# Kernel tuning notes

Measured on AMD Instinct MI355X. Metric: run time of the kernel, lower is better.

The kernel has to match this reference:

```python
import jax, jax.numpy as jnp
import numpy as np

EPS = 1e-5  # PyTorch BatchNorm2d default eps


def _batchnorm(x, gamma, beta):
    # training-mode BN over (N, T, V) per channel; x: [N, C, T, V]
    mean = jnp.mean(x, axis=(0, 2, 3), keepdims=True)
    var = jnp.var(x, axis=(0, 2, 3), keepdims=True)
    inv = jax.lax.rsqrt(var + EPS)
    return (x - mean) * inv * gamma[None, :, None, None] + beta[None, :, None, None]


def setup_inputs() -> dict:
    key = jax.random.key(0)
    ks = jax.random.split(key, 8)
    N, Cin, Cout, T, V, S = 64, 64, 128, 300, 25, 3
    x = jax.random.normal(ks[0], (N, Cin, T, V), dtype=jnp.float32)
    A = jax.random.uniform(ks[1], (S, V, V), dtype=jnp.float32)
    # per-subset 1x1 conv weights/biases (kaiming-ish scale)
    W = jax.random.normal(ks[2], (S, Cout, Cin), dtype=jnp.float32) / np.sqrt(Cin)
    b = jax.random.normal(ks[3], (S, Cout), dtype=jnp.float32) * 0.01
    alpha = jnp.zeros((1,), dtype=jnp.float32)
    bn_gamma = jnp.ones((Cout,), dtype=jnp.float32)
    bn_beta = jnp.zeros((Cout,), dtype=jnp.float32)
    # residual down path (in_channels != out_channels): conv1x1 + BN
    down_W = jax.random.normal(ks[4], (Cout, Cin), dtype=jnp.float32) / np.sqrt(Cin)
    down_b = jax.random.normal(ks[5], (Cout,), dtype=jnp.float32) * 0.01
    down_gamma = jnp.ones((Cout,), dtype=jnp.float32)
    down_beta = jnp.zeros((Cout,), dtype=jnp.float32)
    return {
        "x": x, "A": A, "W": W, "b": b, "alpha": alpha,
        "bn_gamma": bn_gamma, "bn_beta": bn_beta,
        "down_W": down_W, "down_b": down_b,
        "down_gamma": down_gamma, "down_beta": down_beta,
    }


def reference(x, A, W, b, alpha, bn_gamma, bn_beta, down_W, down_b, down_gamma, down_beta):
    V = x.shape[-1]
    eye = jnp.eye(V, dtype=x.dtype)
    A_adj = A + alpha[0] * eye[None]  # [S, V, V]
    # sum_s conv1x1_s( x @ A_s ): fuse adjacency matmul, 1x1 conv, subset sum
    y_agg = jnp.einsum('nctv,svw,soc->notw', x, A_adj, W)
    y_agg = y_agg + jnp.sum(b, axis=0)[None, :, None, None]
    y = _batchnorm(y_agg, bn_gamma, bn_beta)
    # residual down: 1x1 conv + BN (in_channels != out_channels)
    res = jnp.einsum('nctv,oc->notv', x, down_W) + down_b[None, :, None, None]
    res = _batchnorm(res, down_gamma, down_beta)
    return jax.nn.relu(y + res)
```

## Files before the change

### kernel.cpp

```cpp
#include <hip/hip_runtime.h>
#include <hip/hip_bf16.h>

#define N_   64
#define CIN  64
#define COUT 128
#define T_   300
#define V_   25
#define S_   3
#define NTV  (N_ * T_ * V_)

#define TS     10
#define NTB    (T_ / TS)
#define NBLK   (N_ * NTB)
#define RED_ROWS   64
#define RED_BLOCKS (NBLK / RED_ROWS)

#define WS_P    0
#define WS_P2   (WS_P + NBLK * 512)
#define WS_COEF (WS_P2 + RED_BLOCKS * 512)
#define WS_WF   (WS_COEF + 512)
#define WS_WSF  (WS_WF + 16384)
#define WS_AF   (WS_WSF + 16384)

typedef __attribute__((ext_vector_type(8))) short short8;
typedef __attribute__((ext_vector_type(4))) float f32x4;

__device__ __forceinline__ unsigned short bfbits(float f) {
    union { __hip_bfloat16 h; unsigned short u; } cv;
    cv.h = __float2bfloat16(f);
    return cv.u;
}
__device__ __forceinline__ unsigned int pack2(float lo, float hi) {
    return (unsigned int)bfbits(lo) | ((unsigned int)bfbits(hi) << 16);
}

__device__ __forceinline__ int zoff(int nl, int k) {
    int slot = (k >> 3) ^ (nl & 31);
    return nl * 512 + slot * 16 + (k & 7) * 2;
}

__global__ __launch_bounds__(256) void k_prep(const float* __restrict__ W,
                                              const float* __restrict__ dW,
                                              const float* __restrict__ A,
                                              const float* __restrict__ alpha,
                                              unsigned short* __restrict__ Wf,
                                              unsigned short* __restrict__ Af) {
    int i = blockIdx.x * 256 + threadIdx.x;
    {
        int j = i & 7, lane = (i >> 3) & 63, ks = (i >> 9) & 7;
        int of = (i >> 12) & 1, oh = i >> 13;
        int o = oh * 32 + of * 16 + (lane & 15);
        int k = ks * 32 + (lane >> 4) * 8 + j;
        float wv = (k < 192) ? W[(k >> 6) * (COUT * CIN) + o * CIN + (k & 63)]
                             : dW[o * CIN + (k - 192)];
        Wf[i] = bfbits(wv);
    }
    if (i < 4096) {
        int j = i & 7, lane = (i >> 3) & 63, wf = (i >> 9) & 1, s = i >> 10;
        int v = (lane >> 4) * 8 + j, w = wf * 16 + (lane & 15);
        float av;
        if (s < 3)
            av = (v < V_ && w < V_)
                   ? A[(s * V_ + v) * V_ + w] + ((v == w) ? alpha[0] : 0.f)
                   : 0.f;
        else
            av = (v == w && v < V_) ? 1.f : 0.f;
        Af[i] = bfbits(av);
    }
}

__global__ __launch_bounds__(256) void k_prep2(const float* __restrict__ W,
                                               const float* __restrict__ dW,
                                               const float* __restrict__ coef,
                                               unsigned short* __restrict__ Wsf) {
    int i = blockIdx.x * 256 + threadIdx.x;
    int j = i & 7, lane = (i >> 3) & 63, ks = (i >> 9) & 7;
    int of = (i >> 12) & 1, oh = i >> 13;
    int o = oh * 32 + of * 16 + (lane & 15);
    int k = ks * 32 + (lane >> 4) * 8 + j;
    float wv = (k < 192) ? W[(k >> 6) * (COUT * CIN) + o * CIN + (k & 63)]
                         : dW[o * CIN + (k - 192)];
    float sc = (k < 192) ? coef[o] : coef[COUT + o];
    Wsf[i] = bfbits(wv * sc);
}

struct XRaw { f32x4 a0, a1; float s; };

__device__ __forceinline__ XRaw load_raw(const float* __restrict__ base, int lq) {
    XRaw r;
    if (lq < 3) {
        r.a0 = *(const f32x4*)(base + lq * 8);
        r.a1 = *(const f32x4*)(base + lq * 8 + 4);
        r.s = 0.f;
    } else {
        r.s = base[24];
        r.a0 = (f32x4){0.f, 0.f, 0.f, 0.f};
        r.a1 = (f32x4){0.f, 0.f, 0.f, 0.f};
    }
    return r;
}

__device__ __forceinline__ short8 cvt_xfr(const XRaw& x, int lq) {
    short8 r;
    if (lq < 3) {
#pragma unroll
        for (int j = 0; j < 4; ++j) {
            r[j]     = (short)bfbits(x.a0[j]);
            r[4 + j] = (short)bfbits(x.a1[j]);
        }
    } else {
        r[0] = (short)bfbits(x.s);
#pragma unroll
        for (int j = 1; j < 8; ++j) r[j] = 0;
    }
    return r;
}

__device__ __forceinline__ void stage(char* zb, const unsigned short* Alds,
                                      short8 xfr, int oh, int lq, int lr, int lane) {
    const f32x4 zero = {0.f, 0.f, 0.f, 0.f};
#pragma unroll
    for (int s = 0; s < 4; ++s)
#pragma unroll
        for (int wf = 0; wf < 2; ++wf) {
            short8 af = *(const short8*)(Alds + ((s * 2 + wf) * 64 + lane) * 8);
            f32x4 d = __builtin_amdgcn_mfma_f32_16x16x32_bf16(xfr, af, zero, 0, 0, 0);
            unsigned long long pk = (unsigned long long)pack2(d[0], d[1])
                                  | ((unsigned long long)pack2(d[2], d[3]) << 32);
            int row = wf * 16 + lr;
            int k = s * 64 + oh * 16 + lq * 4;
            *(unsigned long long*)(zb + zoff(row, k)) = pk;
        }
}

template<bool STATS, int MINW>
__global__ __launch_bounds__(256, MINW) void k_gemm(
    const float* __restrict__ x, const unsigned short* __restrict__ Wf,
    const unsigned short* __restrict__ Af, const float* __restrict__ coef,
    float* __restrict__ P, float* __restrict__ out)
{
    __shared__ __align__(16) unsigned short Zt[2][32 * 256];
    __shared__ __align__(16) unsigned short Alds[8 * 64 * 8];

    const int tid = threadIdx.x;
    const int oh = tid >> 6, lane = tid & 63;
    const int lq = lane >> 4, lr = lane & 15;

    const int bid = blockIdx.x;
    const int n = bid / NTB, tb = bid % NTB;
    const int t0 = tb * TS;

    for (int i = tid; i < 512; i += 256)
        *(short8*)(Alds + i * 8) = *(const short8*)(Af + i * 8);

    short8 wfr[2][8];
#pragma unroll
    for (int of = 0; of < 2; ++of)
#pragma unroll
        for (int ks = 0; ks < 8; ++ks)
            wfr[of][ks] = *(const short8*)(Wf + (((oh * 2 + of) * 8 + ks) * 64 + lane) * 8);

    float c0v[2] = {0.f, 0.f};
    if (!STATS) {
        c0v[0] = coef[2 * COUT + oh * 32 + lr];
        c0v[1] = coef[2 * COUT + oh * 32 + 16 + lr];
    }

    float sy[2] = {0.f, 0.f}, sy2[2] = {0.f, 0.f};
    float sr[2] = {0.f, 0.f}, sr2[2] = {0.f, 0.f};

    const int c = oh * 16 + lr;
    const float* xrow = x + ((size_t)(n * CIN + c) * T_) * V_;

    __syncthreads();

    {
        XRaw r0 = load_raw(xrow + (size_t)t0 * V_, lq);
        stage((char*)Zt[0], Alds, cvt_xfr(r0, lq), oh, lq, lr, lane);
    }
    XRaw slotA = load_raw(xrow + (size_t)(t0 + 1) * V_, lq);

    const f32x4 zero = {0.f, 0.f, 0.f, 0.f};

    for (int tt = 0; tt < TS; ++tt) {
        const int t = t0 + tt;
        char* zb = (char*)Zt[tt & 1];
        __syncthreads();

        XRaw slotB;
        if (tt + 2 < TS) slotB = load_raw(xrow + (size_t)(t + 2) * V_, lq);
        else { slotB.a0 = zero; slotB.a1 = zero; slotB.s = 0.f; }

        if (tt + 1 < TS)
            stage((char*)Zt[(tt + 1) & 1], Alds, cvt_xfr(slotA, lq), oh, lq, lr, lane);

        f32x4 acc[2][2];

        if constexpr (STATS) {
#pragma unroll
            for (int ks = 6; ks < 8; ++ks) {
                short8 za[2];
                za[0] = *(const short8*)(zb + zoff(lr, ks * 32 + lq * 8));
                za[1] = *(const short8*)(zb + zoff(16 + lr, ks * 32 + lq * 8));
#pragma unroll
                for (int mf = 0; mf < 2; ++mf)
#pragma unroll
                    for (int of = 0; of < 2; ++of)
                        acc[mf][of] = __builtin_amdgcn_mfma_f32_16x16x32_bf16(
                            za[mf], wfr[of][ks], ks == 6 ? zero : acc[mf][of], 0, 0, 0);
            }
#pragma unroll
            for (int of = 0; of < 2; ++of)
#pragma unroll
                for (int mf = 0; mf < 2; ++mf)
#pragma unroll
                    for (int r = 0; r < 4; ++r) {
                        float rv = acc[mf][of][r];
                        sr[of] += rv; sr2[of] = fmaf(rv, rv, sr2[of]);
                    }
#pragma unroll
            for (int ks = 0; ks < 6; ++ks) {
                short8 za[2];
                za[0] = *(const short8*)(zb + zoff(lr, ks * 32 + lq * 8));
                za[1] = *(const short8*)(zb + zoff(16 + lr, ks * 32 + lq * 8));
#pragma unroll
                for (int mf = 0; mf < 2; ++mf)
#pragma unroll
                    for (int of = 0; of < 2; ++of)
                        acc[mf][of] = __builtin_amdgcn_mfma_f32_16x16x32_bf16(
                            za[mf], wfr[of][ks], ks == 0 ? zero : acc[mf][of], 0, 0, 0);
            }
#pragma unroll
            for (int of = 0; of < 2; ++of)
#pragma unroll
                for (int mf = 0; mf < 2; ++mf)
#pragma unroll
                    for (int r = 0; r < 4; ++r) {
                        float yv = acc[mf][of][r];
                        sy[of] += yv; sy2[of] = fmaf(yv, yv, sy2[of]);
                    }
        } else {
#pragma unroll
            for (int ks = 0; ks < 8; ++ks) {
                short8 za[2];
                za[0] = *(const short8*)(zb + zoff(lr, ks * 32 + lq * 8));
                za[1] = *(const short8*)(zb + zoff(16 + lr, ks * 32 + lq * 8));
#pragma unroll
                for (int mf = 0; mf < 2; ++mf)
#pragma unroll
                    for (int of = 0; of < 2; ++of)
                        acc[mf][of] = __builtin_amdgcn_mfma_f32_16x16x32_bf16(
                            za[mf], wfr[of][ks], ks == 0 ? zero : acc[mf][of], 0, 0, 0);
            }
#pragma unroll
            for (int of = 0; of < 2; ++of) {
                int o = oh * 32 + of * 16 + lr;
                float* rowp = out + ((size_t)(n * COUT + o) * T_ + t) * V_;
                f32x4 v0;
#pragma unroll
                for (int r = 0; r < 4; ++r) v0[r] = fmaxf(acc[0][of][r] + c0v[of], 0.f);
                *(f32x4*)(rowp + lq * 4) = v0;
                if (lq < 2) {
                    f32x4 v1;
#pragma unroll
                    for (int r = 0; r < 4; ++r) v1[r] = fmaxf(acc[1][of][r] + c0v[of], 0.f);
                    *(f32x4*)(rowp + 16 + lq * 4) = v1;
                } else if (lq == 2) {
                    rowp[24] = fmaxf(acc[1][of][0] + c0v[of], 0.f);
                }
            }
        }

        slotA.a0 = slotB.a0; slotA.a1 = slotB.a1; slotA.s = slotB.s;
    }

    if constexpr (STATS) {
#pragma unroll
        for (int of = 0; of < 2; ++of) {
            sy[of]  += __shfl_xor(sy[of], 16);  sy[of]  += __shfl_xor(sy[of], 32);
            sy2[of] += __shfl_xor(sy2[of], 16); sy2[of] += __shfl_xor(sy2[of], 32);
            sr[of]  += __shfl_xor(sr[of], 16);  sr[of]  += __shfl_xor(sr[of], 32);
            sr2[of] += __shfl_xor(sr2[of], 16); sr2[of] += __shfl_xor(sr2[of], 32);
        }
        if (lq == 0) {
            float* p = P + (size_t)bid * 512;
#pragma unroll
            for (int of = 0; of < 2; ++of) {
                int o = oh * 32 + of * 16 + lr;
                p[o] = sy[of]; p[128 + o] = sy2[of];
                p[256 + o] = sr[of]; p[384 + o] = sr2[of];
            }
        }
    }
}

__global__ __launch_bounds__(256) void k_red(const float* __restrict__ P,
                                             float* __restrict__ P2) {
    const int tid = threadIdx.x;
    float a0 = 0.f, a1 = 0.f;
    const int row0 = blockIdx.x * RED_ROWS;
    for (int r = 0; r < RED_ROWS; ++r) {
        const float* p = P + (size_t)(row0 + r) * 512;
        a0 += p[tid];
        a1 += p[256 + tid];
    }
    P2[blockIdx.x * 512 + tid] = a0;
    P2[blockIdx.x * 512 + 256 + tid] = a1;
}

__global__ __launch_bounds__(128) void k_coef(
    const float* __restrict__ P2, const float* __restrict__ gamma,
    const float* __restrict__ beta, const float* __restrict__ dgamma,
    const float* __restrict__ dbeta, const float* __restrict__ b,
    const float* __restrict__ db, float* __restrict__ coef) {
    const int o = threadIdx.x;
    float sy = 0.f, sy2 = 0.f, sr = 0.f, sr2 = 0.f;
    for (int r2 = 0; r2 < RED_BLOCKS; ++r2) {
        const float* p = P2 + r2 * 512;
        sy += p[o]; sy2 += p[128 + o]; sr += p[256 + o]; sr2 += p[384 + o];
    }
    const float bsum = b[o] + b[COUT + o] + b[2 * COUT + o];
    const float dbo = db[o];
    float syb  = sy + (float)NTV * bsum;
    float sy2b = sy2 + 2.f * bsum * sy + (float)NTV * bsum * bsum;
    float srb  = sr + (float)NTV * dbo;
    float sr2b = sr2 + 2.f * dbo * sr + (float)NTV * dbo * dbo;
    const float invn = 1.f / (float)NTV;
    float my = syb * invn, mr = srb * invn;
    float vy = fmaf(-my, my, sy2b * invn);
    float vr = fmaf(-mr, mr, sr2b * invn);
    float ay = rsqrtf(vy + 1e-5f) * gamma[o];
    float ar = rsqrtf(vr + 1e-5f) * dgamma[o];
    float c0 = beta[o] - my * ay + dbeta[o] - mr * ar + ay * bsum + ar * dbo;
    coef[o] = ay; coef[COUT + o] = ar; coef[2 * COUT + o] = c0;
}

extern "C" void kernel_launch(void* const* d_in, const int* in_sizes, int n_in,
                              void* d_out, int out_size, void* d_ws, size_t ws_size,
                              hipStream_t stream) {
    const float* x      = (const float*)d_in[0];
    const float* A      = (const float*)d_in[1];
    const float* W      = (const float*)d_in[2];
    const float* b      = (const float*)d_in[3];
    const float* alpha  = (const float*)d_in[4];
    const float* gamma  = (const float*)d_in[5];
    const float* beta   = (const float*)d_in[6];
    const float* dW     = (const float*)d_in[7];
    const float* db     = (const float*)d_in[8];
    const float* dgamma = (const float*)d_in[9];
    const float* dbeta  = (const float*)d_in[10];

    float* ws   = (float*)d_ws;
    float* P    = ws + WS_P;
    float* P2   = ws + WS_P2;
    float* coef = ws + WS_COEF;
    unsigned short* Wf  = (unsigned short*)(ws + WS_WF);
    unsigned short* Wsf = (unsigned short*)(ws + WS_WSF);
    unsigned short* Af  = (unsigned short*)(ws + WS_AF);
    float* out  = (float*)d_out;

    k_prep<<<128, 256, 0, stream>>>(W, dW, A, alpha, Wf, Af);
    k_gemm<true, 3><<<NBLK, 256, 0, stream>>>(x, Wf, Af, nullptr, P, nullptr);
    k_red<<<RED_BLOCKS, 256, 0, stream>>>(P, P2);
    k_coef<<<1, 128, 0, stream>>>(P2, gamma, beta, dgamma, dbeta, b, db, coef);
    k_prep2<<<128, 256, 0, stream>>>(W, dW, coef, Wsf);
    k_gemm<false, 4><<<NBLK, 256, 0, stream>>>(x, Wsf, Af, coef, nullptr, out);
}
```

Measured before the change: 258.4 us.

## Restructure GEMM LDS staging: padded rows, single barrier, A fragments from global

Replaces the XOR-swizzled Z tile with a padded 528-byte row layout and precomputed per-thread read and write bases, so the LDS address maths is simpler. The per-step work is reordered: the next step's staging MFMA and the next x load are issued after the current step's GEMM, with one lgkmcnt-wait-plus-barrier per step. The adjacency fragments are now read from global memory (L2) instead of an LDS copy. bf16 packing uses the paired conversion intrinsic, and the stats kernel's launch bound goes from 3 to 4 waves. The risks are more global or L2 traffic for the A fragments, possible LDS bank conflicts in the padded layout, and register pressure at the higher occupancy target.

```diff
diff --git a/kernel.cpp b/kernel.cpp
--- a/kernel.cpp
+++ b/kernel.cpp
@@ -15,6 +15,8 @@
 #define RED_ROWS   64
 #define RED_BLOCKS (NBLK / RED_ROWS)
 
+#define ROWB   528
+
 #define WS_P    0
 #define WS_P2   (WS_P + NBLK * 512)
 #define WS_COEF (WS_P2 + RED_BLOCKS * 512)
@@ -25,19 +27,19 @@
 typedef __attribute__((ext_vector_type(8))) short short8;
 typedef __attribute__((ext_vector_type(4))) float f32x4;
 
+#define LDS_BARRIER() asm volatile("s_waitcnt lgkmcnt(0)\n\ts_barrier" ::: "memory")
+
 __device__ __forceinline__ unsigned short bfbits(float f) {
     union { __hip_bfloat16 h; unsigned short u; } cv;
     cv.h = __float2bfloat16(f);
     return cv.u;
 }
 __device__ __forceinline__ unsigned int pack2(float lo, float hi) {
-    return (unsigned int)bfbits(lo) | ((unsigned int)bfbits(hi) << 16);
-}
-
-__device__ __forceinline__ int zoff(int nl, int k) {
-    int slot = (k >> 3) ^ (nl & 31);
-    return nl * 512 + slot * 16 + (k & 7) * 2;
-}
+    union { __hip_bfloat162 h2; unsigned int u; } cv;
+    cv.h2 = __float22bfloat162_rn(float2{lo, hi});
+    return cv.u;
+}
+
 
 __global__ __launch_bounds__(256) void k_prep(const float* __restrict__ W,
                                               const float* __restrict__ dW,
@@ -101,46 +103,41 @@
 }
 
 __device__ __forceinline__ short8 cvt_xfr(const XRaw& x, int lq) {
-    short8 r;
+    union { short8 s8; unsigned int u[4]; } b;
     if (lq < 3) {
-#pragma unroll
-        for (int j = 0; j < 4; ++j) {
-            r[j]     = (short)bfbits(x.a0[j]);
-            r[4 + j] = (short)bfbits(x.a1[j]);
-        }
+        b.u[0] = pack2(x.a0[0], x.a0[1]);
+        b.u[1] = pack2(x.a0[2], x.a0[3]);
+        b.u[2] = pack2(x.a1[0], x.a1[1]);
+        b.u[3] = pack2(x.a1[2], x.a1[3]);
     } else {
-        r[0] = (short)bfbits(x.s);
-#pragma unroll
-        for (int j = 1; j < 8; ++j) r[j] = 0;
-    }
-    return r;
-}
-
-__device__ __forceinline__ void stage(char* zb, const unsigned short* Alds,
-                                      short8 xfr, int oh, int lq, int lr, int lane) {
+        b.u[0] = pack2(x.s, 0.f);
+        b.u[1] = 0; b.u[2] = 0; b.u[3] = 0;
+    }
+    return b.s8;
+}
+
+__device__ __forceinline__ void stage(char* zwr, const unsigned short* __restrict__ Af,
+                                      short8 xfr, int lane) {
     const f32x4 zero = {0.f, 0.f, 0.f, 0.f};
 #pragma unroll
     for (int s = 0; s < 4; ++s)
 #pragma unroll
         for (int wf = 0; wf < 2; ++wf) {
-            short8 af = *(const short8*)(Alds + ((s * 2 + wf) * 64 + lane) * 8);
+            short8 af = *(const short8*)(Af + ((s * 2 + wf) * 64 + lane) * 8);
             f32x4 d = __builtin_amdgcn_mfma_f32_16x16x32_bf16(xfr, af, zero, 0, 0, 0);
             unsigned long long pk = (unsigned long long)pack2(d[0], d[1])
                                   | ((unsigned long long)pack2(d[2], d[3]) << 32);
-            int row = wf * 16 + lr;
-            int k = s * 64 + oh * 16 + lq * 4;
-            *(unsigned long long*)(zb + zoff(row, k)) = pk;
+            *(unsigned long long*)(zwr + (wf * 16 * ROWB + s * 32)) = pk;
         }
 }
 
-template<bool STATS, int MINW>
-__global__ __launch_bounds__(256, MINW) void k_gemm(
+template<bool STATS>
+__global__ __launch_bounds__(256, 4) void k_gemm(
     const float* __restrict__ x, const unsigned short* __restrict__ Wf,
     const unsigned short* __restrict__ Af, const float* __restrict__ coef,
     float* __restrict__ P, float* __restrict__ out)
 {
-    __shared__ __align__(16) unsigned short Zt[2][32 * 256];
-    __shared__ __align__(16) unsigned short Alds[8 * 64 * 8];
+    __shared__ __align__(16) char Zt[2][32 * ROWB];
 
     const int tid = threadIdx.x;
     const int oh = tid >> 6, lane = tid & 63;
@@ -149,9 +146,6 @@
     const int bid = blockIdx.x;
     const int n = bid / NTB, tb = bid % NTB;
     const int t0 = tb * TS;
-
-    for (int i = tid; i < 512; i += 256)
-        *(short8*)(Alds + i * 8) = *(const short8*)(Af + i * 8);
 
     short8 wfr[2][8];
 #pragma unroll
@@ -172,11 +166,13 @@
     const int c = oh * 16 + lr;
     const float* xrow = x + ((size_t)(n * CIN + c) * T_) * V_;
 
-    __syncthreads();
+    const int base_rd = lr * ROWB + lq * 128;
+    const int base_wr = lr * ROWB + (oh & 1) * 256 + (lq >> 1) * 128
+                      + (lq & 1) * 8 + (oh >> 1) * 16;
 
     {
         XRaw r0 = load_raw(xrow + (size_t)t0 * V_, lq);
-        stage((char*)Zt[0], Alds, cvt_xfr(r0, lq), oh, lq, lr, lane);
+        stage((char*)Zt[0] + base_wr, Af, cvt_xfr(r0, lq), lane);
     }
     XRaw slotA = load_raw(xrow + (size_t)(t0 + 1) * V_, lq);
 
@@ -184,15 +180,8 @@
 
     for (int tt = 0; tt < TS; ++tt) {
         const int t = t0 + tt;
-        char* zb = (char*)Zt[tt & 1];
-        __syncthreads();
-
-        XRaw slotB;
-        if (tt + 2 < TS) slotB = load_raw(xrow + (size_t)(t + 2) * V_, lq);
-        else { slotB.a0 = zero; slotB.a1 = zero; slotB.s = 0.f; }
-
-        if (tt + 1 < TS)
-            stage((char*)Zt[(tt + 1) & 1], Alds, cvt_xfr(slotA, lq), oh, lq, lr, lane);
+        const char* zb = (const char*)Zt[tt & 1] + base_rd;
+        LDS_BARRIER();
 
         f32x4 acc[2][2];
 
@@ -200,8 +189,8 @@
 #pragma unroll
             for (int ks = 6; ks < 8; ++ks) {
                 short8 za[2];
-                za[0] = *(const short8*)(zb + zoff(lr, ks * 32 + lq * 8));
-                za[1] = *(const short8*)(zb + zoff(16 + lr, ks * 32 + lq * 8));
+                za[0] = *(const short8*)(zb + ks * 16);
+                za[1] = *(const short8*)(zb + 16 * ROWB + ks * 16);
 #pragma unroll
                 for (int mf = 0; mf < 2; ++mf)
 #pragma unroll
@@ -221,8 +210,8 @@
 #pragma unroll
             for (int ks = 0; ks < 6; ++ks) {
                 short8 za[2];
-                za[0] = *(const short8*)(zb + zoff(lr, ks * 32 + lq * 8));
-                za[1] = *(const short8*)(zb + zoff(16 + lr, ks * 32 + lq * 8));
+                za[0] = *(const short8*)(zb + ks * 16);
+                za[1] = *(const short8*)(zb + 16 * ROWB + ks * 16);
 #pragma unroll
                 for (int mf = 0; mf < 2; ++mf)
 #pragma unroll
@@ -230,6 +219,10 @@
                         acc[mf][of] = __builtin_amdgcn_mfma_f32_16x16x32_bf16(
                             za[mf], wfr[of][ks], ks == 0 ? zero : acc[mf][of], 0, 0, 0);
             }
+            if (tt + 1 < TS)
+                stage((char*)Zt[(tt + 1) & 1] + base_wr, Af, cvt_xfr(slotA, lq), lane);
+            if (tt + 2 < TS)
+                slotA = load_raw(xrow + (size_t)(t + 2) * V_, lq);
 #pragma unroll
             for (int of = 0; of < 2; ++of)
 #pragma unroll
@@ -243,8 +236,8 @@
 #pragma unroll
             for (int ks = 0; ks < 8; ++ks) {
                 short8 za[2];
-                za[0] = *(const short8*)(zb + zoff(lr, ks * 32 + lq * 8));
-                za[1] = *(const short8*)(zb + zoff(16 + lr, ks * 32 + lq * 8));
+                za[0] = *(const short8*)(zb + ks * 16);
+                za[1] = *(const short8*)(zb + 16 * ROWB + ks * 16);
 #pragma unroll
                 for (int mf = 0; mf < 2; ++mf)
 #pragma unroll
@@ -252,6 +245,11 @@
                         acc[mf][of] = __builtin_amdgcn_mfma_f32_16x16x32_bf16(
                             za[mf], wfr[of][ks], ks == 0 ? zero : acc[mf][of], 0, 0, 0);
             }
+            if (tt + 1 < TS)
+                stage((char*)Zt[(tt + 1) & 1] + base_wr, Af, cvt_xfr(slotA, lq), lane);
+            if (tt + 2 < TS)
+                slotA = load_raw(xrow + (size_t)(t + 2) * V_, lq);
+
 #pragma unroll
             for (int of = 0; of < 2; ++of) {
                 int o = oh * 32 + of * 16 + lr;
@@ -270,8 +268,6 @@
                 }
             }
         }
-
-        slotA.a0 = slotB.a0; slotA.a1 = slotB.a1; slotA.s = slotB.s;
     }
 
     if constexpr (STATS) {
@@ -360,9 +356,9 @@
     float* out  = (float*)d_out;
 
     k_prep<<<128, 256, 0, stream>>>(W, dW, A, alpha, Wf, Af);
-    k_gemm<true, 3><<<NBLK, 256, 0, stream>>>(x, Wf, Af, nullptr, P, nullptr);
+    k_gemm<true><<<NBLK, 256, 0, stream>>>(x, Wf, Af, nullptr, P, nullptr);
     k_red<<<RED_BLOCKS, 256, 0, stream>>>(P, P2);
     k_coef<<<1, 128, 0, stream>>>(P2, gamma, beta, dgamma, dbeta, b, db, coef);
     k_prep2<<<128, 256, 0, stream>>>(W, dW, coef, Wsf);
-    k_gemm<false, 4><<<NBLK, 256, 0, stream>>>(x, Wsf, Af, coef, nullptr, out);
-}
+    k_gemm<false><<<NBLK, 256, 0, stream>>>(x, Wsf, Af, coef, nullptr, out);
+}
```

Result: slower. 357.2 us (+38.2%).
